# Optimization experiments

Hardware: AMD Instinct MI355X
Metric: run time of the kernel (lower is better)

Reference implementation:

```python
import jax, jax.numpy as jnp
import numpy as np

PI = np.pi

def dct_2_1d(x):
    # DCT-II over last dim, norm=None, matching the torch FFT-based impl.
    N = x.shape[-1]
    v = jnp.concatenate([x[..., ::2], jnp.flip(x[..., 1::2], axis=-1)], axis=-1)
    Vc = jnp.fft.fft(v, axis=-1)
    k = -jnp.arange(N, dtype=x.dtype) * PI / (2 * N)
    V = Vc.real * jnp.cos(k) - Vc.imag * jnp.sin(k)
    return 2 * V

def idct_2_1d(X):
    # Inverse of dct_2_1d (scaled DCT-III), norm=None.
    N = X.shape[-1]
    X_v = X / 2
    k = jnp.arange(N, dtype=X.dtype) * PI / (2 * N)
    W_r, W_i = jnp.cos(k), jnp.sin(k)
    V_t_r = X_v
    V_t_i = jnp.concatenate([jnp.zeros_like(X_v[..., :1]), -jnp.flip(X_v, axis=-1)[..., :-1]], axis=-1)
    V_r = V_t_r * W_r - V_t_i * W_i
    V_i = V_t_r * W_i + V_t_i * W_r
    # torch.fft.irfft(complex, n=N) uses the first N//2+1 entries; numpy/jax irfft crops the same way.
    v = jnp.fft.irfft(V_r + 1j * V_i, n=N, axis=-1)
    x = jnp.zeros_like(v)
    x = x.at[..., ::2].set(v[..., :N - N // 2])
    x = x.at[..., 1::2].set(jnp.flip(v, axis=-1)[..., :N // 2])
    return x

def setup_inputs() -> dict:
    key = jax.random.key(0)
    k1, k2 = jax.random.split(key)
    B, N, C = 256, 196, 768  # N = h*w = 14*14, C = dim
    x = jax.random.normal(k1, (B, N, C), dtype=jnp.float32)
    weight = jax.random.normal(k2, (C, N), dtype=jnp.float32) * 0.02
    return {"x": x, "weight": weight}

def reference(x, weight):
    # x: [B, N, C]; weight: [C, N]
    xt = jnp.transpose(x, (0, 2, 1)).astype(jnp.float32)  # [B, C, N]
    X = dct_2_1d(xt)
    X = X * weight  # broadcast [C, N] over batch
    y = idct_2_1d(X)
    return jnp.transpose(y, (0, 2, 1))  # [B, N, C]
```

## Files before the change

### kernel.cpp

```cpp
#include <hip/hip_runtime.h>
#include <stdint.h>

typedef __bf16 bf16;
typedef __bf16 bf16x8 __attribute__((ext_vector_type(8)));
typedef __bf16 bf16x4 __attribute__((ext_vector_type(4)));
typedef float f32x4 __attribute__((ext_vector_type(4)));

#define N_DIM 196
#define C_DIM 768
#define B_DIM 256
#define KSTEPS 7
#define MT1 14
#define MT2 13
#define CT 64
#define LPITCH 232
#define NWAVES 8

#define D2F_ELEMS (MT1 * KSTEPS * 512)
#define EF_ELEMS  (MT2 * KSTEPS * 512)

__global__ void init_mats(bf16* __restrict__ d2f, bf16* __restrict__ ef) {
    int idx = blockIdx.x * 256 + threadIdx.x;
    const float PI = 3.14159265358979323846f;
    if (idx < D2F_ELEMS) {
        int j    = idx & 7;
        int lane = (idx >> 3) & 63;
        int rest = idx >> 9;
        int ks = rest % KSTEPS;
        int mt = rest / KSTEPS;
        int row = mt * 16 + (lane & 15);
        int col = ks * 32 + (lane >> 4) * 8 + j;
        float v = 0.0f;
        if (row < N_DIM && col < N_DIM) {
            int t = ((2 * col + 1) * row) % (4 * N_DIM);
            v = 2.0f * cosf(PI * (float)t / (float)(2 * N_DIM));
        }
        d2f[idx] = (bf16)v;
    } else {
        int e = idx - D2F_ELEMS;
        if (e < EF_ELEMS) {
            int j    = e & 7;
            int lane = (e >> 3) & 63;
            int rest = e >> 9;
            int ks = rest % KSTEPS;
            int mt = rest / KSTEPS;
            int row = mt * 16 + (lane & 15);
            int col = ks * 32 + (lane >> 4) * 8 + j;
            float v = 0.0f;
            if (row < N_DIM && col < N_DIM) {
                if (col == 0) {
                    v = 1.0f / (float)(2 * N_DIM);
                } else {
                    int t = ((2 * row + 1) * col) % (4 * N_DIM);
                    v = cosf(PI * (float)t / (float)(2 * N_DIM)) / (float)N_DIM;
                }
            }
            ef[e] = (bf16)v;
        }
    }
}

#define TRRD(dst, a, imm) \
    asm volatile("ds_read_b64_tr_b16 %0, %1 offset:" #imm : "=v"(dst) : "v"(a))

__global__ __launch_bounds__(512, 4) void dct_fused(
        const float* __restrict__ x, const float* __restrict__ wgt,
        const bf16* __restrict__ d2f, const bf16* __restrict__ ef,
        float* __restrict__ out) {
    __shared__ bf16 lds[CT * LPITCH];

    const int b  = blockIdx.y;
    const int c0 = blockIdx.x * CT;
    const int t  = threadIdx.x;
    const int wave = t >> 6;
    const int lane = t & 63;
    const int ln15 = lane & 15;
    const int q    = lane >> 4;

    {
        const int cg8 = t & 7;
        const int mr  = t >> 3;
        const float* xp = x + (size_t)b * N_DIM * C_DIM + c0 + cg8 * 8;
#pragma unroll
        for (int i = 0; i < 3; ++i) {
            int m = i * 64 + mr;
            float4 v0 = *(const float4*)(xp + (size_t)m * C_DIM);
            float4 v1 = *(const float4*)(xp + (size_t)m * C_DIM + 4);
            bf16x8 pv;
            pv[0] = (bf16)v0.x; pv[1] = (bf16)v0.y; pv[2] = (bf16)v0.z; pv[3] = (bf16)v0.w;
            pv[4] = (bf16)v1.x; pv[5] = (bf16)v1.y; pv[6] = (bf16)v1.z; pv[7] = (bf16)v1.w;
            *(bf16x8*)(lds + ((m >> 2) * 4 + (cg8 >> 1)) * 64 + (m & 3) * 16 + (cg8 & 1) * 8) = pv;
        }
        {
            int m = 192 + mr;
            if (m < 224) {
                float4 v0 = make_float4(0.f, 0.f, 0.f, 0.f);
                float4 v1 = v0;
                if (m < N_DIM) {
                    v0 = *(const float4*)(xp + (size_t)m * C_DIM);
                    v1 = *(const float4*)(xp + (size_t)m * C_DIM + 4);
                }
                bf16x8 pv;
                pv[0] = (bf16)v0.x; pv[1] = (bf16)v0.y; pv[2] = (bf16)v0.z; pv[3] = (bf16)v0.w;
                pv[4] = (bf16)v1.x; pv[5] = (bf16)v1.y; pv[6] = (bf16)v1.z; pv[7] = (bf16)v1.w;
                *(bf16x8*)(lds + ((m >> 2) * 4 + (cg8 >> 1)) * 64 + (m & 3) * 16 + (cg8 & 1) * 8) = pv;
            }
        }
    }
    __syncthreads();

    f32x4 acc[2][4] = {};
    {
        const uint32_t xaddr = (uint32_t)(size_t)&lds[0] + q * 1024 + ln15 * 8;
#pragma unroll
        for (int ks = 0; ks < KSTEPS; ++ks) {
            uint32_t a = xaddr + ks * 4096;
            bf16x4 l0, l1, l2, l3, h0, h1, h2, h3;
            TRRD(l0, a, 0);   TRRD(h0, a, 512);
            TRRD(l1, a, 128); TRRD(h1, a, 640);
            TRRD(l2, a, 256); TRRD(h2, a, 768);
            TRRD(l3, a, 384); TRRD(h3, a, 896);
            bf16x8 afr[2];
#pragma unroll
            for (int ml = 0; ml < 2; ++ml) {
                int mt = wave + 8 * ml;
                if (mt < MT1)
                    afr[ml] = *(const bf16x8*)(d2f + ((size_t)(mt * KSTEPS + ks) * 64 + lane) * 8);
            }
            asm volatile("s_waitcnt lgkmcnt(0)");
            __builtin_amdgcn_sched_barrier(0);
            bf16x8 bb[4];
            bb[0] = __builtin_shufflevector(l0, h0, 0, 1, 2, 3, 4, 5, 6, 7);
            bb[1] = __builtin_shufflevector(l1, h1, 0, 1, 2, 3, 4, 5, 6, 7);
            bb[2] = __builtin_shufflevector(l2, h2, 0, 1, 2, 3, 4, 5, 6, 7);
            bb[3] = __builtin_shufflevector(l3, h3, 0, 1, 2, 3, 4, 5, 6, 7);
#pragma unroll
            for (int ml = 0; ml < 2; ++ml) {
                int mt = wave + 8 * ml;
                if (mt < MT1) {
#pragma unroll
                    for (int ct = 0; ct < 4; ++ct)
                        acc[ml][ct] = __builtin_amdgcn_mfma_f32_16x16x32_bf16(
                            afr[ml], bb[ct], acc[ml][ct], 0, 0, 0);
                }
            }
        }
    }
    __syncthreads();

#pragma unroll
    for (int ml = 0; ml < 2; ++ml) {
        int mt = wave + 8 * ml;
        if (mt >= MT1) continue;
        int kb = mt * 16 + q * 4;
#pragma unroll
        for (int ct = 0; ct < 4; ++ct) {
            int cc = ct * 16 + ln15;
            float4 wv = make_float4(0.f, 0.f, 0.f, 0.f);
            if (kb < N_DIM)
                wv = *(const float4*)(wgt + (size_t)(c0 + cc) * N_DIM + kb);
            bf16x4 pv;
            pv[0] = (bf16)(acc[ml][ct][0] * wv.x);
            pv[1] = (bf16)(acc[ml][ct][1] * wv.y);
            pv[2] = (bf16)(acc[ml][ct][2] * wv.z);
            pv[3] = (bf16)(acc[ml][ct][3] * wv.w);
            *(bf16x4*)(lds + cc * LPITCH + kb) = pv;
        }
    }
    __syncthreads();

    f32x4 acc2[2][4] = {};
#pragma unroll
    for (int ks = 0; ks < KSTEPS; ++ks) {
        bf16x8 afr2[4];
#pragma unroll
        for (int ct = 0; ct < 4; ++ct)
            afr2[ct] = *(const bf16x8*)(lds + (ct * 16 + ln15) * LPITCH + ks * 32 + q * 8);
#pragma unroll
        for (int i = 0; i < 2; ++i) {
            int nt = wave + 8 * i;
            if (nt < MT2) {
                bf16x8 bfr = *(const bf16x8*)(ef + ((size_t)(nt * KSTEPS + ks) * 64 + lane) * 8);
#pragma unroll
                for (int ct = 0; ct < 4; ++ct)
                    acc2[i][ct] = __builtin_amdgcn_mfma_f32_16x16x32_bf16(
                        afr2[ct], bfr, acc2[i][ct], 0, 0, 0);
            }
        }
    }

#pragma unroll
    for (int i = 0; i < 2; ++i) {
        int nt = wave + 8 * i;
        if (nt >= MT2) continue;
        int n = nt * 16 + ln15;
        if (n < N_DIM) {
#pragma unroll
            for (int ct = 0; ct < 4; ++ct)
                *(f32x4*)(out + ((size_t)b * N_DIM + n) * C_DIM + c0 + ct * 16 + q * 4) =
                    acc2[i][ct];
        }
    }
}

extern "C" void kernel_launch(void* const* d_in, const int* in_sizes, int n_in,
                              void* d_out, int out_size, void* d_ws, size_t ws_size,
                              hipStream_t stream) {
    const float* x   = (const float*)d_in[0];
    const float* wgt = (const float*)d_in[1];
    float* out = (float*)d_out;

    bf16* d2f = (bf16*)d_ws;
    bf16* ef  = d2f + D2F_ELEMS;

    int tot = D2F_ELEMS + EF_ELEMS;
    init_mats<<<(tot + 255) / 256, 256, 0, stream>>>(d2f, ef);

    dim3 grid(C_DIM / CT, B_DIM);
    dct_fused<<<grid, 512, 0, stream>>>(x, wgt, d2f, ef, out);
}
```

Before: 302.9 us.

## Use 16 waves per block, one M-tile per wave, separate LDS buffers

Doubles the block to 1024 threads so each wave owns a single 16-row tile in both DCT GEMM stages instead of looping over two. The weighted intermediate now goes to its own LDS region, so the barrier between the first GEMM and the weighted store is removed. The input load per thread drops from four rows to two. In exchange, LDS per block grows and the 1024-thread blocks may limit occupancy, and waves 14-15 idle in both GEMMs.

```diff
diff --git a/kernel.cpp b/kernel.cpp
--- a/kernel.cpp
+++ b/kernel.cpp
@@ -14,7 +14,7 @@
 #define MT2 13
 #define CT 64
 #define LPITCH 232
-#define NWAVES 8
+#define XELEMS 14336
 
 #define D2F_ELEMS (MT1 * KSTEPS * 512)
 #define EF_ELEMS  (MT2 * KSTEPS * 512)
@@ -63,11 +63,11 @@
 #define TRRD(dst, a, imm) \
     asm volatile("ds_read_b64_tr_b16 %0, %1 offset:" #imm : "=v"(dst) : "v"(a))
 
-__global__ __launch_bounds__(512, 4) void dct_fused(
+__global__ __launch_bounds__(1024, 8) void dct_fused(
         const float* __restrict__ x, const float* __restrict__ wgt,
         const bf16* __restrict__ d2f, const bf16* __restrict__ ef,
         float* __restrict__ out) {
-    __shared__ bf16 lds[CT * LPITCH];
+    __shared__ bf16 lds[XELEMS + CT * LPITCH];
 
     const int b  = blockIdx.y;
     const int c0 = blockIdx.x * CT;
@@ -77,13 +77,14 @@
     const int ln15 = lane & 15;
     const int q    = lane >> 4;
 
+    bf16* const lds_t1w = lds + XELEMS;
+
     {
         const int cg8 = t & 7;
         const int mr  = t >> 3;
         const float* xp = x + (size_t)b * N_DIM * C_DIM + c0 + cg8 * 8;
-#pragma unroll
-        for (int i = 0; i < 3; ++i) {
-            int m = i * 64 + mr;
+        {
+            int m = mr;
             float4 v0 = *(const float4*)(xp + (size_t)m * C_DIM);
             float4 v1 = *(const float4*)(xp + (size_t)m * C_DIM + 4);
             bf16x8 pv;
@@ -92,7 +93,7 @@
             *(bf16x8*)(lds + ((m >> 2) * 4 + (cg8 >> 1)) * 64 + (m & 3) * 16 + (cg8 & 1) * 8) = pv;
         }
         {
-            int m = 192 + mr;
+            int m = 128 + mr;
             if (m < 224) {
                 float4 v0 = make_float4(0.f, 0.f, 0.f, 0.f);
                 float4 v1 = v0;
@@ -109,8 +110,8 @@
     }
     __syncthreads();
 
-    f32x4 acc[2][4] = {};
-    {
+    f32x4 acc[4] = {};
+    if (wave < MT1) {
         const uint32_t xaddr = (uint32_t)(size_t)&lds[0] + q * 1024 + ln15 * 8;
 #pragma unroll
         for (int ks = 0; ks < KSTEPS; ++ks) {
@@ -120,13 +121,7 @@
             TRRD(l1, a, 128); TRRD(h1, a, 640);
             TRRD(l2, a, 256); TRRD(h2, a, 768);
             TRRD(l3, a, 384); TRRD(h3, a, 896);
-            bf16x8 afr[2];
-#pragma unroll
-            for (int ml = 0; ml < 2; ++ml) {
-                int mt = wave + 8 * ml;
-                if (mt < MT1)
-                    afr[ml] = *(const bf16x8*)(d2f + ((size_t)(mt * KSTEPS + ks) * 64 + lane) * 8);
-            }
+            bf16x8 afr = *(const bf16x8*)(d2f + ((size_t)(wave * KSTEPS + ks) * 64 + lane) * 8);
             asm volatile("s_waitcnt lgkmcnt(0)");
             __builtin_amdgcn_sched_barrier(0);
             bf16x8 bb[4];
@@ -135,24 +130,11 @@
             bb[2] = __builtin_shufflevector(l2, h2, 0, 1, 2, 3, 4, 5, 6, 7);
             bb[3] = __builtin_shufflevector(l3, h3, 0, 1, 2, 3, 4, 5, 6, 7);
 #pragma unroll
-            for (int ml = 0; ml < 2; ++ml) {
-                int mt = wave + 8 * ml;
-                if (mt < MT1) {
-#pragma unroll
-                    for (int ct = 0; ct < 4; ++ct)
-                        acc[ml][ct] = __builtin_amdgcn_mfma_f32_16x16x32_bf16(
-                            afr[ml], bb[ct], acc[ml][ct], 0, 0, 0);
-                }
-            }
+            for (int ct = 0; ct < 4; ++ct)
+                acc[ct] = __builtin_amdgcn_mfma_f32_16x16x32_bf16(afr, bb[ct], acc[ct], 0, 0, 0);
         }
-    }
-    __syncthreads();
 
-#pragma unroll
-    for (int ml = 0; ml < 2; ++ml) {
-        int mt = wave + 8 * ml;
-        if (mt >= MT1) continue;
-        int kb = mt * 16 + q * 4;
+        int kb = wave * 16 + q * 4;
 #pragma unroll
         for (int ct = 0; ct < 4; ++ct) {
             int cc = ct * 16 + ln15;
@@ -160,45 +142,39 @@
             if (kb < N_DIM)
                 wv = *(const float4*)(wgt + (size_t)(c0 + cc) * N_DIM + kb);
             bf16x4 pv;
-            pv[0] = (bf16)(acc[ml][ct][0] * wv.x);
-            pv[1] = (bf16)(acc[ml][ct][1] * wv.y);
-            pv[2] = (bf16)(acc[ml][ct][2] * wv.z);
-            pv[3] = (bf16)(acc[ml][ct][3] * wv.w);
-            *(bf16x4*)(lds + cc * LPITCH + kb) = pv;
+            pv[0] = (bf16)(acc[ct][0] * wv.x);
+            pv[1] = (bf16)(acc[ct][1] * wv.y);
+            pv[2] = (bf16)(acc[ct][2] * wv.z);
+            pv[3] = (bf16)(acc[ct][3] * wv.w);
+            *(bf16x4*)(lds_t1w + cc * LPITCH + kb) = pv;
         }
     }
     __syncthreads();
 
-    f32x4 acc2[2][4] = {};
-#pragma unroll
-    for (int ks = 0; ks < KSTEPS; ++ks) {
-        bf16x8 afr2[4];
+    if (wave < MT2) {
 #pragma unroll
         for (int ct = 0; ct < 4; ++ct)
-            afr2[ct] = *(const bf16x8*)(lds + (ct * 16 + ln15) * LPITCH + ks * 32 + q * 8);
 #pragma unroll
-        for (int i = 0; i < 2; ++i) {
-            int nt = wave + 8 * i;
-            if (nt < MT2) {
-                bf16x8 bfr = *(const bf16x8*)(ef + ((size_t)(nt * KSTEPS + ks) * 64 + lane) * 8);
+            for (int r = 0; r < 4; ++r)
+                acc[ct][r] = 0.0f;
 #pragma unroll
-                for (int ct = 0; ct < 4; ++ct)
-                    acc2[i][ct] = __builtin_amdgcn_mfma_f32_16x16x32_bf16(
-                        afr2[ct], bfr, acc2[i][ct], 0, 0, 0);
-            }
+        for (int ks = 0; ks < KSTEPS; ++ks) {
+            bf16x8 afr2[4];
+#pragma unroll
+            for (int ct = 0; ct < 4; ++ct)
+                afr2[ct] = *(const bf16x8*)(lds_t1w + (ct * 16 + ln15) * LPITCH + ks * 32 + q * 8);
+            bf16x8 bfr = *(const bf16x8*)(ef + ((size_t)(wave * KSTEPS + ks) * 64 + lane) * 8);
+#pragma unroll
+            for (int ct = 0; ct < 4; ++ct)
+                acc[ct] = __builtin_amdgcn_mfma_f32_16x16x32_bf16(afr2[ct], bfr, acc[ct], 0, 0, 0);
         }
-    }
 
-#pragma unroll
-    for (int i = 0; i < 2; ++i) {
-        int nt = wave + 8 * i;
-        if (nt >= MT2) continue;
-        int n = nt * 16 + ln15;
+        int n = wave * 16 + ln15;
         if (n < N_DIM) {
 #pragma unroll
             for (int ct = 0; ct < 4; ++ct)
                 *(f32x4*)(out + ((size_t)b * N_DIM + n) * C_DIM + c0 + ct * 16 + q * 4) =
-                    acc2[i][ct];
+                    acc[ct];
         }
     }
 }
@@ -217,5 +193,5 @@
     init_mats<<<(tot + 255) / 256, 256, 0, stream>>>(d2f, ef);
 
     dim3 grid(C_DIM / CT, B_DIM);
-    dct_fused<<<grid, 512, 0, stream>>>(x, wgt, d2f, ef, out);
+    dct_fused<<<grid, 1024, 0, stream>>>(x, wgt, d2f, ef, out);
 }
```

Result: faster. 293.0 us (-3.3%).
